# Performance work log

Measured on AMD Instinct MI355X. Metric: run time of the kernel, lower is better.

The kernel has to match this reference:

```python
import jax, jax.numpy as jnp
import numpy as np

DIM = 1024
NUM_HEADS = 16
HEAD_DIM = DIM // NUM_HEADS
SCALE = HEAD_DIM ** (-0.5)


def alibi_slopes(num_heads):
    x = (2 ** 8) ** (1.0 / num_heads)
    return jnp.array([1.0 / x ** (i + 1) for i in range(num_heads)], dtype=jnp.float32)


def setup_inputs() -> dict:
    key = jax.random.key(0)
    ks = jax.random.split(key, 6)
    B, N = 2, 2048
    x = jax.random.normal(ks[0], (B, N, DIM), dtype=jnp.float32)
    s = DIM ** -0.5
    Wq = jax.random.normal(ks[1], (DIM, DIM), dtype=jnp.float32) * s
    Wk = jax.random.normal(ks[2], (DIM, DIM), dtype=jnp.float32) * s
    Wv = jax.random.normal(ks[3], (DIM, DIM), dtype=jnp.float32) * s
    Wp = jax.random.normal(ks[4], (DIM, DIM), dtype=jnp.float32) * s
    bp = jnp.zeros((DIM,), dtype=jnp.float32)
    return {"x": x, "Wq": Wq, "Wk": Wk, "Wv": Wv, "Wp": Wp, "bp": bp}


def reference(x, Wq, Wk, Wv, Wp, bp):
    B, N, C = x.shape
    H, D = NUM_HEADS, HEAD_DIM
    # Linear layers use torch convention: y = x @ W.T
    q = (x @ Wq.T).reshape(B, N, H, D).transpose(0, 2, 1, 3)  # [B,H,N,D]
    k = (x @ Wk.T).reshape(B, N, H, D).transpose(0, 2, 1, 3)
    v = (x @ Wv.T).reshape(B, N, H, D).transpose(0, 2, 1, 3)
    # ALiBi bias: slopes[h] * (j - i), shape [H,N,N]
    rel = (jnp.arange(N)[None, :] - jnp.arange(N)[:, None]).astype(jnp.float32)
    bias = alibi_slopes(H)[:, None, None] * rel  # [H,N,N]
    # NOTE: original code DIVIDES by scale (= head_dim**-0.5), i.e. multiplies by sqrt(D)
    score = jnp.einsum("bhnd,bhmd->bhnm", q, k) / SCALE + bias[None]
    attn = jax.nn.softmax(score, axis=-1)
    out = jnp.einsum("bhnm,bhmd->bhnd", attn, v)
    out = out.transpose(0, 2, 1, 3).reshape(B, N, C)
    return out @ Wp.T + bp
```

## Files before the change

kernel.cpp:

```cpp
#include <hip/hip_runtime.h>
#include <hip/hip_bf16.h>
#include <cstdint>
#include <cstddef>

#define BB 2
#define NN 2048
#define CC 1024
#define HH 16
#define DD 64
#define MM (BB*NN)

typedef __attribute__((ext_vector_type(8))) _Float16 half8;
typedef __attribute__((ext_vector_type(4))) _Float16 half4;
typedef __attribute__((ext_vector_type(4))) float f32x4;

__device__ __forceinline__ float exp2_fast(float x) {
    float r; asm("v_exp_f32 %0, %1" : "=v"(r) : "v"(x)); return r;
}

__device__ __forceinline__ void gl_lds16(const void* g, void* l) {
    __builtin_amdgcn_global_load_lds(
        (const __attribute__((address_space(1))) unsigned int*)g,
        (__attribute__((address_space(3))) unsigned int*)l, 16, 0, 0);
}

__global__ __launch_bounds__(256) void cvtAll(
    const float* __restrict__ x, const float* __restrict__ wq,
    const float* __restrict__ wk, const float* __restrict__ wv,
    const float* __restrict__ wp, _Float16* __restrict__ X16,
    _Float16* __restrict__ W16) {
    const int NX4 = MM * CC / 4;
    const int NW4 = CC * CC / 4;
    int i = blockIdx.x * 256 + threadIdx.x;
    const float4* src;
    half4* dst;
    if (i < NX4) {
        src = (const float4*)x + i;
        dst = (half4*)X16 + i;
    } else {
        int j = i - NX4;
        int s = j >> 18, off = j & (NW4 - 1);
        const float* wsel = (s == 0) ? wq : (s == 1) ? wk : (s == 2) ? wv : wp;
        src = (const float4*)wsel + off;
        dst = (half4*)(W16 + (size_t)s * CC * CC) + off;
    }
    float4 v = *src;
    half4 h = { (_Float16)v.x, (_Float16)v.y, (_Float16)v.z, (_Float16)v.w };
    *dst = h;
}

__global__ __launch_bounds__(256) void gemmQKV(
    const _Float16* __restrict__ A, const _Float16* __restrict__ B,
    _Float16* __restrict__ QH, _Float16* __restrict__ KH,
    _Float16* __restrict__ VT, float qscale) {
    __shared__ _Float16 sA[128 * 64];
    __shared__ _Float16 sB[128 * 64];
    const int K = CC;

    const int t = threadIdx.x;
    const int bm = blockIdx.y, bn = blockIdx.x;
    const int w = t >> 6, lane = t & 63;
    const int wr = (w >> 1) * 64, wc = (w & 1) * 64;
    const int lr = lane & 15, lg = lane >> 4;

    f32x4 acc[4][4];
#pragma unroll
    for (int a = 0; a < 4; ++a)
#pragma unroll
        for (int b2 = 0; b2 < 4; ++b2)
#pragma unroll
            for (int e = 0; e < 4; ++e) acc[a][b2][e] = 0.f;

    for (int kt = 0; kt < K; kt += 64) {
#pragma unroll
        for (int p = 0; p < 4; ++p) {
            int u = p * 256 + t;
            int rowu = u >> 3, su = (u & 7) ^ (rowu & 7);
            gl_lds16(A + (size_t)(bm * 128 + rowu) * K + kt + su * 8, sA + u * 8);
            gl_lds16(B + (size_t)(bn * 128 + rowu) * K + kt + su * 8, sB + u * 8);
        }
        __syncthreads();

#pragma unroll
        for (int c = 0; c < 2; ++c) {
            half8 af[4], bf[4];
#pragma unroll
            for (int f = 0; f < 4; ++f) {
                int ra = wr + f * 16 + lr;
                af[f] = *(const half8*)((const char*)sA + ((ra * 128 + c * 64 + lg * 16) ^ ((ra & 7) << 4)));
                int rb = wc + f * 16 + lr;
                bf[f] = *(const half8*)((const char*)sB + ((rb * 128 + c * 64 + lg * 16) ^ ((rb & 7) << 4)));
            }
#pragma unroll
            for (int fi = 0; fi < 4; ++fi)
#pragma unroll
                for (int fj = 0; fj < 4; ++fj)
                    acc[fi][fj] = __builtin_amdgcn_mfma_f32_16x16x32_f16(af[fi], bf[fj], acc[fi][fj], 0, 0, 0);
        }
        __syncthreads();
    }

#pragma unroll
    for (int fi = 0; fi < 4; ++fi)
#pragma unroll
        for (int fj = 0; fj < 4; ++fj) {
            int col = bn * 128 + wc + fj * 16 + lr;
            int sel = col >> 10, c10 = col & 1023;
            int h2 = c10 >> 6, d2 = c10 & 63;
            int rowb = bm * 128 + wr + fi * 16 + lg * 4;
            int b2 = rowb >> 11, n2 = rowb & (NN - 1);
            if (sel == 0) {
#pragma unroll
                for (int e = 0; e < 4; ++e)
                    QH[((size_t)(b2 * HH + h2) * NN + n2 + e) * DD + d2] =
                        (_Float16)(acc[fi][fj][e] * qscale);
            } else if (sel == 1) {
#pragma unroll
                for (int e = 0; e < 4; ++e)
                    KH[((size_t)(b2 * HH + h2) * NN + n2 + e) * DD + d2] =
                        (_Float16)acc[fi][fj][e];
            } else {
                half4 pk = { (_Float16)acc[fi][fj][0], (_Float16)acc[fi][fj][1],
                             (_Float16)acc[fi][fj][2], (_Float16)acc[fi][fj][3] };
                *(half4*)(VT + ((size_t)(b2 * HH + h2) * DD + d2) * NN + n2) = pk;
            }
        }
}

__global__ __launch_bounds__(256) void gemmPROJ(
    const _Float16* __restrict__ A, const _Float16* __restrict__ B,
    const float* __restrict__ bias, float* __restrict__ Cout) {
    __shared__ _Float16 sA[128 * 64];
    __shared__ _Float16 sB[64 * 64];
    const int K = CC, N = CC;

    const int t = threadIdx.x;
    const int bm = blockIdx.y, bn = blockIdx.x;
    const int w = t >> 6, lane = t & 63;
    const int wr = (w >> 1) * 64, wc = (w & 1) * 32;
    const int lr = lane & 15, lg = lane >> 4;

    f32x4 acc[4][2];
#pragma unroll
    for (int a = 0; a < 4; ++a)
#pragma unroll
        for (int b2 = 0; b2 < 2; ++b2)
#pragma unroll
            for (int e = 0; e < 4; ++e) acc[a][b2][e] = 0.f;

    for (int kt = 0; kt < K; kt += 64) {
#pragma unroll
        for (int p = 0; p < 4; ++p) {
            int u = p * 256 + t;
            int rowu = u >> 3, su = (u & 7) ^ (rowu & 7);
            gl_lds16(A + (size_t)(bm * 128 + rowu) * K + kt + su * 8, sA + u * 8);
        }
#pragma unroll
        for (int p = 0; p < 2; ++p) {
            int u = p * 256 + t;
            int rowu = u >> 3, su = (u & 7) ^ (rowu & 7);
            gl_lds16(B + (size_t)(bn * 64 + rowu) * K + kt + su * 8, sB + u * 8);
        }
        __syncthreads();

#pragma unroll
        for (int c = 0; c < 2; ++c) {
            half8 af[4], bf[2];
#pragma unroll
            for (int f = 0; f < 4; ++f) {
                int ra = wr + f * 16 + lr;
                af[f] = *(const half8*)((const char*)sA + ((ra * 128 + c * 64 + lg * 16) ^ ((ra & 7) << 4)));
            }
#pragma unroll
            for (int f = 0; f < 2; ++f) {
                int rb = wc + f * 16 + lr;
                bf[f] = *(const half8*)((const char*)sB + ((rb * 128 + c * 64 + lg * 16) ^ ((rb & 7) << 4)));
            }
#pragma unroll
            for (int fi = 0; fi < 4; ++fi)
#pragma unroll
                for (int fj = 0; fj < 2; ++fj)
                    acc[fi][fj] = __builtin_amdgcn_mfma_f32_16x16x32_f16(af[fi], bf[fj], acc[fi][fj], 0, 0, 0);
        }
        __syncthreads();
    }

#pragma unroll
    for (int fi = 0; fi < 4; ++fi)
#pragma unroll
        for (int fj = 0; fj < 2; ++fj)
#pragma unroll
            for (int e = 0; e < 4; ++e) {
                int row = bm * 128 + wr + fi * 16 + lg * 4 + e;
                int col = bn * 64 + wc + fj * 16 + lr;
                Cout[(size_t)row * N + col] = acc[fi][fj][e] + bias[col];
            }
}

__global__ __launch_bounds__(256) void attn16(
    const _Float16* __restrict__ Qh, const _Float16* __restrict__ Kh,
    const _Float16* __restrict__ Vt, _Float16* __restrict__ AO) {
    __shared__ _Float16 sK[2][64 * 64];
    __shared__ _Float16 sV[2][64 * 64];

    const int t = threadIdx.x, w = t >> 6, lane = t & 63;
    const int lr = lane & 15, lg = lane >> 4;
    const int qb = blockIdx.x, bh = blockIdx.y;
    const int b = bh >> 4, h = bh & 15;
    const int i0 = qb * 64;
    const size_t baseND = (size_t)bh * NN * DD;
    const size_t baseDN = (size_t)bh * DD * NN;

    half8 qf[2];
    {
        const size_t qoff = baseND + (size_t)(i0 + w * 16 + lr) * DD;
        qf[0] = *(const half8*)(Qh + qoff + 0 * 32 + lg * 8);
        qf[1] = *(const half8*)(Qh + qoff + 1 * 32 + lg * 8);
    }

    f32x4 accO[4];
#pragma unroll
    for (int e = 0; e < 4; ++e)
        accO[e][0] = accO[e][1] = accO[e][2] = accO[e][3] = 0.f;
    float m_run = -INFINITY, l_run = 0.f;

    const float slope2 = exp2f(-0.5f * (float)(h + 1)) * 1.44269504f;
    const float s64 = slope2 * 64.f;
    f32x4 cini[4];
#pragma unroll
    for (int ct = 0; ct < 4; ++ct)
#pragma unroll
        for (int e = 0; e < 4; ++e)
            cini[ct][e] = slope2 * (float)(ct * 16 + lg * 4 + e);

    auto stage = [&](int buf, int jt) {
#pragma unroll
        for (int p = 0; p < 2; ++p) {
            int u = p * 256 + t;
            int rowu = u >> 3, su = (u & 7) ^ (rowu & 7);
            gl_lds16(Kh + baseND + (size_t)(jt * 64 + rowu) * DD + su * 8, &sK[buf][u * 8]);
            gl_lds16(Vt + baseDN + (size_t)rowu * NN + jt * 64 + su * 8, &sV[buf][u * 8]);
        }
    };

    stage(0, 0);
    __syncthreads();
    int cur = 0;
    float tb = 0.f;

    for (int jt = 0; jt < NN / 64; ++jt) {
        if (jt + 1 < NN / 64) stage(cur ^ 1, jt + 1);

        f32x4 s[4];
#pragma unroll
        for (int ct = 0; ct < 4; ++ct) s[ct] = cini[ct];

        __builtin_amdgcn_s_setprio(1);
#pragma unroll
        for (int ct = 0; ct < 4; ++ct)
#pragma unroll
            for (int c = 0; c < 2; ++c) {
                int row = ct * 16 + lr;
                half8 kf = *(const half8*)((const char*)&sK[cur][0] +
                    ((row * 128 + c * 64 + lg * 16) ^ ((row & 7) << 4)));
                s[ct] = __builtin_amdgcn_mfma_f32_16x16x32_f16(kf, qf[c], s[ct], 0, 0, 0);
            }
        __builtin_amdgcn_s_setprio(0);

        float x0 = fmaxf(fmaxf(s[0][0], s[0][1]), fmaxf(s[0][2], s[0][3]));
        float x1 = fmaxf(fmaxf(s[1][0], s[1][1]), fmaxf(s[1][2], s[1][3]));
        float x2 = fmaxf(fmaxf(s[2][0], s[2][1]), fmaxf(s[2][2], s[2][3]));
        float x3 = fmaxf(fmaxf(s[3][0], s[3][1]), fmaxf(s[3][2], s[3][3]));
        float mx = fmaxf(fmaxf(x0, x1), fmaxf(x2, x3));
        mx = fmaxf(mx, __shfl_xor(mx, 16, 64));
        mx = fmaxf(mx, __shfl_xor(mx, 32, 64));
        float mxt = mx + tb;
        float mnew = fmaxf(m_run, mxt);
        float al = exp2_fast(m_run - mnew);
        float msh = mnew - tb;
        m_run = mnew;
#pragma unroll
        for (int ct = 0; ct < 4; ++ct)
#pragma unroll
            for (int e = 0; e < 4; ++e) s[ct][e] = exp2_fast(s[ct][e] - msh);
        float y0 = (s[0][0] + s[0][1]) + (s[0][2] + s[0][3]);
        float y1 = (s[1][0] + s[1][1]) + (s[1][2] + s[1][3]);
        float y2 = (s[2][0] + s[2][1]) + (s[2][2] + s[2][3]);
        float y3 = (s[3][0] + s[3][1]) + (s[3][2] + s[3][3]);
        float sum = (y0 + y1) + (y2 + y3);
        sum += __shfl_xor(sum, 16, 64);
        sum += __shfl_xor(sum, 32, 64);
        l_run = l_run * al + sum;

        half4 pf[4];
#pragma unroll
        for (int ct = 0; ct < 4; ++ct) {
            half4 pk = { (_Float16)s[ct][0], (_Float16)s[ct][1],
                         (_Float16)s[ct][2], (_Float16)s[ct][3] };
            pf[ct] = pk;
        }

#pragma unroll
        for (int ctd = 0; ctd < 4; ++ctd)
#pragma unroll
            for (int e = 0; e < 4; ++e) accO[ctd][e] *= al;

        __builtin_amdgcn_s_setprio(1);
#pragma unroll
        for (int ctd = 0; ctd < 4; ++ctd) {
            int row = ctd * 16 + lr;
#pragma unroll
            for (int ct = 0; ct < 4; ++ct) {
                half4 vf = *(const half4*)((const char*)&sV[cur][0] +
                    ((row * 128 + ct * 32 + lg * 8) ^ ((row & 7) << 4)));
                accO[ctd] = __builtin_amdgcn_mfma_f32_16x16x16f16(vf, pf[ct], accO[ctd], 0, 0, 0);
            }
        }
        __builtin_amdgcn_s_setprio(0);

        __syncthreads();
        cur ^= 1;
        tb += s64;
    }

    float rl = 1.0f / l_run;
    const size_t obase = ((size_t)b * NN + i0 + w * 16 + lr) * CC + h * DD;
#pragma unroll
    for (int ctd = 0; ctd < 4; ++ctd) {
        half4 ov = { (_Float16)(accO[ctd][0] * rl), (_Float16)(accO[ctd][1] * rl),
                     (_Float16)(accO[ctd][2] * rl), (_Float16)(accO[ctd][3] * rl) };
        *(half4*)(AO + obase + ctd * 16 + lg * 4) = ov;
    }
}

extern "C" void kernel_launch(void* const* d_in, const int* in_sizes, int n_in,
                              void* d_out, int out_size, void* d_ws, size_t ws_size,
                              hipStream_t stream) {
    const float* x  = (const float*)d_in[0];
    const float* Wq = (const float*)d_in[1];
    const float* Wk = (const float*)d_in[2];
    const float* Wv = (const float*)d_in[3];
    const float* Wp = (const float*)d_in[4];
    const float* bp = (const float*)d_in[5];
    float* out = (float*)d_out;

    char* ws = (char*)d_ws;
    const size_t MB = 1024 * 1024;
    _Float16* X16 = (_Float16*)(ws + 0 * MB);
    _Float16* W16 = (_Float16*)(ws + 8 * MB);
    _Float16* QH  = (_Float16*)(ws + 16 * MB);
    _Float16* KH  = (_Float16*)(ws + 24 * MB);
    _Float16* VT  = (_Float16*)(ws + 32 * MB);
    _Float16* AO  = (_Float16*)(ws + 40 * MB);
    _Float16* WP16 = W16 + 3 * 1024 * 1024;

    cvtAll<<<8192, 256, 0, stream>>>(x, Wq, Wk, Wv, Wp, X16, W16);

    const float QSCALE = 8.0f * 1.44269504f;
    gemmQKV<<<dim3(3 * CC / 128, MM / 128), 256, 0, stream>>>(X16, W16, QH, KH, VT, QSCALE);

    attn16<<<dim3(NN / 64, BB * HH), 256, 0, stream>>>(QH, KH, VT, AO);

    gemmPROJ<<<dim3(CC / 64, MM / 128), 256, 0, stream>>>(AO, WP16, bp, out);
}
```

Baseline: 157.1 us.

## Use 16x16x32 MFMA for PV via LDS P staging, remap XCD blocks

The attention PV product now packs P to fp16 with cvt_pkrtz and writes it to a per-wave LDS buffer. It reads P back in the layout that lets the wider 16x16x32 MFMA replace the 16x16x16 one, which halves the PV MFMA count. Both GEMMs remap block indices so that consecutive blocks landing on the same XCD share row tiles, aiming for better L2 reuse. The attention grid is transposed so that blocks with the same head are spread across XCDs. Routing P through LDS adds extra LDS traffic and round-toward-zero conversion, which slightly changes rounding.

```diff
diff --git a/kernel.cpp b/kernel.cpp
--- a/kernel.cpp
+++ b/kernel.cpp
@@ -12,6 +12,7 @@
 
 typedef __attribute__((ext_vector_type(8))) _Float16 half8;
 typedef __attribute__((ext_vector_type(4))) _Float16 half4;
+typedef __attribute__((ext_vector_type(2))) _Float16 half2v;
 typedef __attribute__((ext_vector_type(4))) float f32x4;
 
 __device__ __forceinline__ float exp2_fast(float x) {
@@ -58,7 +59,10 @@
     const int K = CC;
 
     const int t = threadIdx.x;
-    const int bm = blockIdx.y, bn = blockIdx.x;
+    const int id = blockIdx.y * gridDim.x + blockIdx.x;
+    const int xcd = id & 7, kk = id >> 3;
+    const int bm = xcd * 4 + (kk & 3);
+    const int bn = kk >> 2;
     const int w = t >> 6, lane = t & 63;
     const int wr = (w >> 1) * 64, wc = (w & 1) * 64;
     const int lr = lane & 15, lg = lane >> 4;
@@ -135,7 +139,10 @@
     const int K = CC, N = CC;
 
     const int t = threadIdx.x;
-    const int bm = blockIdx.y, bn = blockIdx.x;
+    const int id = blockIdx.y * gridDim.x + blockIdx.x;
+    const int xcd = id & 7, kk = id >> 3;
+    const int bm = xcd * 4 + (kk & 3);
+    const int bn = kk >> 2;
     const int w = t >> 6, lane = t & 63;
     const int wr = (w >> 1) * 64, wc = (w & 1) * 32;
     const int lr = lane & 15, lg = lane >> 4;
@@ -202,10 +209,11 @@
     const _Float16* __restrict__ Vt, _Float16* __restrict__ AO) {
     __shared__ _Float16 sK[2][64 * 64];
     __shared__ _Float16 sV[2][64 * 64];
+    __shared__ _Float16 sP[4][16 * 64];
 
     const int t = threadIdx.x, w = t >> 6, lane = t & 63;
     const int lr = lane & 15, lg = lane >> 4;
-    const int qb = blockIdx.x, bh = blockIdx.y;
+    const int bh = blockIdx.x, qb = blockIdx.y;
     const int b = bh >> 4, h = bh & 15;
     const int i0 = qb * 64;
     const size_t baseND = (size_t)bh * NN * DD;
@@ -252,19 +260,17 @@
         if (jt + 1 < NN / 64) stage(cur ^ 1, jt + 1);
 
         f32x4 s[4];
-#pragma unroll
-        for (int ct = 0; ct < 4; ++ct) s[ct] = cini[ct];
-
         __builtin_amdgcn_s_setprio(1);
 #pragma unroll
-        for (int ct = 0; ct < 4; ++ct)
-#pragma unroll
-            for (int c = 0; c < 2; ++c) {
-                int row = ct * 16 + lr;
-                half8 kf = *(const half8*)((const char*)&sK[cur][0] +
-                    ((row * 128 + c * 64 + lg * 16) ^ ((row & 7) << 4)));
-                s[ct] = __builtin_amdgcn_mfma_f32_16x16x32_f16(kf, qf[c], s[ct], 0, 0, 0);
-            }
+        for (int ct = 0; ct < 4; ++ct) {
+            int row = ct * 16 + lr;
+            half8 kf0 = *(const half8*)((const char*)&sK[cur][0] +
+                ((row * 128 + 0 * 64 + lg * 16) ^ ((row & 7) << 4)));
+            half8 kf1 = *(const half8*)((const char*)&sK[cur][0] +
+                ((row * 128 + 1 * 64 + lg * 16) ^ ((row & 7) << 4)));
+            s[ct] = __builtin_amdgcn_mfma_f32_16x16x32_f16(kf0, qf[0], cini[ct], 0, 0, 0);
+            s[ct] = __builtin_amdgcn_mfma_f32_16x16x32_f16(kf1, qf[1], s[ct], 0, 0, 0);
+        }
         __builtin_amdgcn_s_setprio(0);
 
         float x0 = fmaxf(fmaxf(s[0][0], s[0][1]), fmaxf(s[0][2], s[0][3]));
@@ -292,12 +298,14 @@
         sum += __shfl_xor(sum, 32, 64);
         l_run = l_run * al + sum;
 
-        half4 pf[4];
 #pragma unroll
         for (int ct = 0; ct < 4; ++ct) {
-            half4 pk = { (_Float16)s[ct][0], (_Float16)s[ct][1],
-                         (_Float16)s[ct][2], (_Float16)s[ct][3] };
-            pf[ct] = pk;
+            unsigned plo = __builtin_bit_cast(unsigned,
+                __builtin_amdgcn_cvt_pkrtz(s[ct][0], s[ct][1]));
+            unsigned phi = __builtin_bit_cast(unsigned,
+                __builtin_amdgcn_cvt_pkrtz(s[ct][2], s[ct][3]));
+            uint2 pk = { plo, phi };
+            *(uint2*)((char*)sP[w] + ((lr * 128 + ct * 32 + lg * 8) ^ ((lr & 7) << 4))) = pk;
         }
 
 #pragma unroll
@@ -305,17 +313,18 @@
 #pragma unroll
             for (int e = 0; e < 4; ++e) accO[ctd][e] *= al;
 
+        half8 pb0 = *(const half8*)((const char*)sP[w] + ((lr * 128 + 0 * 64 + lg * 16) ^ ((lr & 7) << 4)));
+        half8 pb1 = *(const half8*)((const char*)sP[w] + ((lr * 128 + 1 * 64 + lg * 16) ^ ((lr & 7) << 4)));
         __builtin_amdgcn_s_setprio(1);
 #pragma unroll
-        for (int ctd = 0; ctd < 4; ++ctd) {
-            int row = ctd * 16 + lr;
-#pragma unroll
-            for (int ct = 0; ct < 4; ++ct) {
-                half4 vf = *(const half4*)((const char*)&sV[cur][0] +
-                    ((row * 128 + ct * 32 + lg * 8) ^ ((row & 7) << 4)));
-                accO[ctd] = __builtin_amdgcn_mfma_f32_16x16x16f16(vf, pf[ct], accO[ctd], 0, 0, 0);
-            }
-        }
+        for (int ctd = 0; ctd < 4; ++ctd)
+#pragma unroll
+            for (int c = 0; c < 2; ++c) {
+                int row = ctd * 16 + lr;
+                half8 vf = *(const half8*)((const char*)&sV[cur][0] +
+                    ((row * 128 + c * 64 + lg * 16) ^ ((row & 7) << 4)));
+                accO[ctd] = __builtin_amdgcn_mfma_f32_16x16x32_f16(vf, c ? pb1 : pb0, accO[ctd], 0, 0, 0);
+            }
         __builtin_amdgcn_s_setprio(0);
 
         __syncthreads();
@@ -359,7 +368,7 @@
     const float QSCALE = 8.0f * 1.44269504f;
     gemmQKV<<<dim3(3 * CC / 128, MM / 128), 256, 0, stream>>>(X16, W16, QH, KH, VT, QSCALE);
 
-    attn16<<<dim3(NN / 64, BB * HH), 256, 0, stream>>>(QH, KH, VT, AO);
+    attn16<<<dim3(BB * HH, NN / 64), 256, 0, stream>>>(QH, KH, VT, AO);
 
     gemmPROJ<<<dim3(CC / 64, MM / 128), 256, 0, stream>>>(AO, WP16, bp, out);
 }
```

Result: no change. 155.0 us (-1.3%).
